# Kernel optimization log

Measured on AMD Instinct MI355X. Metric: run time of the kernel, lower is better.

Reference implementation:

```python
import jax, jax.numpy as jnp
import numpy as np

D_MODEL = 512; D_STATE = 32; D_HEAD = 64; G = 4; R = 2
D_INNER = 2 * D_MODEL            # expand=2 -> 1024
H = D_INNER // D_HEAD            # 16 heads
RATIO = H // G                   # 4 heads per group
CHUNK = 128; EPS = 1e-5
DIM_Z = D_INNER; DIM_X = D_INNER
DIM_B = G * D_STATE * R; DIM_C = DIM_B
D_PROJ = DIM_Z + DIM_X + DIM_B + DIM_C + G + G
BATCH = 1; SEQ = 2048


def setup_inputs() -> dict:
    key = jax.random.key(0)
    ks = jax.random.split(key, 10)
    u = jax.random.normal(ks[0], (BATCH, SEQ, D_MODEL), jnp.float32)
    W_in = jax.random.normal(ks[1], (D_MODEL, D_PROJ), jnp.float32) * 0.02
    b_in = jnp.zeros((D_PROJ,), jnp.float32)
    # dt bias init: inverse-softplus of log-uniform dt in [1e-3, 1e-1]
    dt0 = jnp.exp(jax.random.uniform(ks[2], (G,)) * (np.log(0.1) - np.log(0.001)) + np.log(0.001))
    inv_dt = dt0 + jnp.log(-jnp.expm1(-dt0))
    s = DIM_Z + DIM_X + DIM_B + DIM_C
    b_in = b_in.at[s:s + G].set(inv_dt).at[s + G:].set(-3.0)
    W_xup = jax.random.normal(ks[3], (D_HEAD, D_HEAD * R), jnp.float32) * (1.0 / np.sqrt(D_HEAD * R))
    W_ydown = jax.random.normal(ks[4], (D_HEAD * R, D_HEAD), jnp.float32) * (1.0 / np.sqrt(D_HEAD * R))
    A_log = jnp.log(jax.random.uniform(ks[5], (G,), minval=1.0, maxval=16.0))
    theta_log = jax.random.normal(ks[6], (G, D_STATE // 2), jnp.float32)
    D_param = jnp.ones((H,), jnp.float32)
    wB = jnp.ones((D_STATE * R,), jnp.float32)
    wC = jnp.ones((D_STATE * R,), jnp.float32)
    bias_B = jnp.ones((G, D_STATE, R), jnp.float32)
    bias_C = jnp.ones((G, D_STATE, R), jnp.float32)
    W_out = jax.random.normal(ks[7], (D_INNER, D_MODEL), jnp.float32) * 0.02
    return dict(u=u, W_in=W_in, b_in=b_in, W_xup=W_xup, W_ydown=W_ydown,
                A_log=A_log, theta_log=theta_log, D_param=D_param,
                wB=wB, wC=wC, bias_B=bias_B, bias_C=bias_C, W_out=W_out)


def rmsnorm(x, w):
    return x * jax.lax.rsqrt(jnp.mean(x * x, -1, keepdims=True) + EPS) * w


def apply_rope(x, angles):
    # x: (B,L,G,N,R)  angles: (B,L,G,N/2)  -- rotate (even, odd) pairs along N
    Bz, L, Gg, N, Rr = x.shape
    xr = x.reshape(Bz, L, Gg, N // 2, 2, Rr)
    re, im = xr[..., 0, :], xr[..., 1, :]
    c = jnp.cos(angles)[..., None]
    s = jnp.sin(angles)[..., None]
    out = jnp.stack([re * c - im * s, re * s + im * c], axis=-2)
    return out.reshape(Bz, L, Gg, N, Rr)


def segsum(x):
    # x: (..., T) log-decay -> (..., T, T) causal pairwise cumulative sums
    T = x.shape[-1]
    cs = jnp.cumsum(x, -1)
    seg = cs[..., :, None] - cs[..., None, :]
    mask = jnp.tril(jnp.ones((T, T), bool))
    return jnp.where(mask, seg, -jnp.inf)


def chunk_parallel_scan(u_in, dt, A, C):
    # u_in: (B,L,H,N,P)  dt: (B,L,H)  A: (H,)  C: (B,L,H,N,R)
    Bz, L, Hh, N, P = u_in.shape
    Rr = C.shape[-1]
    nc = L // CHUNK
    la = (dt * A).reshape(Bz, nc, CHUNK, Hh)                       # log alpha per chunk
    uc = u_in.reshape(Bz, nc, CHUNK, Hh, N, P)
    Cc = C.reshape(Bz, nc, CHUNK, Hh, N, Rr)
    Lm = jnp.exp(segsum(la.transpose(0, 1, 3, 2)))                 # (B,nc,H,cs,cs)
    h_intra = jnp.einsum('bchts,bcshnp->bcthnp', Lm, uc)           # intra-chunk states
    y_diag = jnp.einsum('bcthnp,bcthnr->bcthpr', h_intra, Cc)
    decay_chunk = jnp.exp(la.sum(2))                               # (B,nc,H)
    h_final = h_intra[:, :, -1]                                    # (B,nc,H,N,P)
    h0 = jnp.zeros((Bz, Hh, N, P), u_in.dtype)

    def step(h, inp):
        d, c = inp
        return h * d[..., None, None] + c, h

    h_last, h_states = jax.lax.scan(
        step, h0, (decay_chunk.transpose(1, 0, 2), h_final.transpose(1, 0, 2, 3, 4)))
    h_states = h_states.transpose(1, 0, 2, 3, 4)                   # state entering each chunk
    decay_intra = jnp.exp(jnp.cumsum(la, 2))                       # (B,nc,cs,H)
    C_scaled = Cc * decay_intra[..., None, None]
    y_off = jnp.einsum('bchnp,bcthnr->bcthpr', h_states, C_scaled)
    y = (y_diag + y_off).reshape(Bz, L, Hh, P, Rr)
    return y, h_last


def _forward(u, W_in, b_in, W_xup, W_ydown, A_log, theta_log, D_param, wB, wC, bias_B, bias_C, W_out):
    Bz, L, _ = u.shape
    N, P = D_STATE, D_HEAD
    proj = u @ W_in + b_in
    o = 0
    z = proj[..., o:o + DIM_Z]; o += DIM_Z
    x = proj[..., o:o + DIM_X]; o += DIM_X
    Bi = proj[..., o:o + DIM_B]; o += DIM_B
    Ci = proj[..., o:o + DIM_C]; o += DIM_C
    dt_raw = proj[..., o:o + G]; o += G
    lam_raw = proj[..., o:o + G]

    dt = jax.nn.softplus(dt_raw)                                   # (B,L,G)
    lam = jax.nn.sigmoid(lam_raw)                                  # trapezoidal coeff
    x = jax.nn.silu(x)

    Bm = rmsnorm(Bi.reshape(Bz, L, G, N * R), wB).reshape(Bz, L, G, N, R) + bias_B
    Cm = rmsnorm(Ci.reshape(Bz, L, G, N * R), wC).reshape(Bz, L, G, N, R) + bias_C

    # data-dependent RoPE: cumulative angles = cumsum_t(dt_t * theta)
    theta = jnp.exp(theta_log)                                     # (G, N/2)
    angles = jnp.cumsum(dt[..., None] * theta, axis=1)             # (B,L,G,N/2)
    Br = apply_rope(Bm, angles)
    Cr = apply_rope(Cm, angles)

    # expand group-shared dynamics to heads
    Bh = jnp.repeat(Br, RATIO, axis=2)                             # (B,L,H,N,R)
    Ch = jnp.repeat(Cr, RATIO, axis=2)
    dth = jnp.repeat(dt, RATIO, axis=2)                            # (B,L,H)
    lamh = jnp.repeat(lam, RATIO, axis=2)
    Ah = jnp.repeat(-jnp.exp(A_log), RATIO)                        # (H,)

    xh = x.reshape(Bz, L, H, P)
    x_up = (xh @ W_xup).reshape(Bz, L, H, P, R)                    # MIMO up-projection
    u_ssm = jnp.einsum('blhnr,blhpr->blhnp', Bh, x_up) * dth[..., None, None]
    # generalized trapezoidal rule: blend current and previous input contribution
    u_prev = jnp.pad(u_ssm[:, :-1], ((0, 0), (1, 0), (0, 0), (0, 0), (0, 0)))
    w = lamh[..., None, None]
    u_trap = w * u_ssm + (1.0 - w) * u_prev

    y, _h = chunk_parallel_scan(u_trap, dth, Ah, Ch)               # (B,L,H,P,R)
    y = y.reshape(Bz, L, H, P * R) @ W_ydown                       # MIMO down-projection
    y = y + D_param[None, None, :, None] * xh                      # skip connection
    y = y * jax.nn.silu(z.reshape(Bz, L, H, P))                    # gate
    return (y.reshape(Bz, L, D_INNER)) @ W_out


def reference(u, W_in, b_in, W_xup, W_ydown, A_log, theta_log, D_param, wB, wC, bias_B, bias_C, W_out):
    return _forward(u, W_in, b_in, W_xup, W_ydown, A_log, theta_log,
                    D_param, wB, wC, bias_B, bias_C, W_out)
```

## Files before the change

kernel.cpp:

```cpp
#include <hip/hip_runtime.h>
#include <hip/hip_bf16.h>

typedef __hip_bfloat16 bf16;
typedef __bf16 bfv8 __attribute__((ext_vector_type(8)));
typedef float fv4 __attribute__((ext_vector_type(4)));

__device__ __forceinline__ float bf2f(bf16 x){ return __bfloat162float(x); }
__device__ __forceinline__ bf16 f2bf(float x){ return __float2bfloat16(x); }
__device__ __forceinline__ float blo(unsigned u){ return __uint_as_float(u<<16); }
__device__ __forceinline__ float bhi(unsigned u){ return __uint_as_float(u & 0xffff0000u); }
struct __align__(8) bf4v { bf16 x,y,z,w; };
struct __align__(16) bf8s { ushort u[8]; };
__device__ __forceinline__ float4 ldb4(const bf16* p){
  ushort4 u = *(const ushort4*)p;
  float4 r;
  r.x = __uint_as_float(((unsigned)u.x)<<16);
  r.y = __uint_as_float(((unsigned)u.y)<<16);
  r.z = __uint_as_float(((unsigned)u.z)<<16);
  r.w = __uint_as_float(((unsigned)u.w)<<16);
  return r;
}
__device__ __forceinline__ void stb4(bf16* p, float4 v){
  bf4v t; t.x=f2bf(v.x); t.y=f2bf(v.y); t.z=f2bf(v.z); t.w=f2bf(v.w);
  *(bf4v*)p = t;
}

#define L_SEQ 2048
#define DPROJ 2568
#define NCHUNK 16
#define TCH 128

__device__ __forceinline__ void tbody(const float* __restrict__ in, bf16* __restrict__ out,
                                      int R, int C, int Cpad, int bx, int by, float (*t)[33])
{
  int c0 = bx*32, r0 = by*32;
  int tx = threadIdx.x & 31, ty = threadIdx.x >> 5;
  for (int i=0;i<32;i+=8){
    int r = r0+i+ty, cc = c0+tx;
    t[i+ty][tx] = (r<R && cc<C) ? in[(size_t)r*C+cc] : 0.f;
  }
  __syncthreads();
  for (int i=0;i<32;i+=8){
    int cc = c0+i+ty, r = r0+tx;
    if (cc<Cpad && r<R) out[(size_t)cc*R + r] = f2bf(t[tx][i+ty]);
  }
}

__global__ void prep(const float* __restrict__ u, bf16* __restrict__ ubf,
                     const float* __restrict__ Win, bf16* __restrict__ WinT,
                     const float* __restrict__ Wout, bf16* __restrict__ WoutT,
                     const float* __restrict__ Wyd, bf16* __restrict__ WydT,
                     const float* __restrict__ Wxup, bf16* __restrict__ WxupT)
{
  __shared__ float t[32][33];
  int b = blockIdx.x;
  if (b < 1024){
    int i = (b*256 + threadIdx.x)*4;
    float4 v = *(const float4*)&u[i];
    stb4(&ubf[i], v);
  } else if (b < 2368){
    int idx = b - 1024;
    tbody(Win, WinT, 512, DPROJ, 2688, idx%84, idx/84, t);
  } else if (b < 2880){
    int idx = b - 2368;
    tbody(Wout, WoutT, 1024, 512, 512, idx%16, idx/16, t);
  } else if (b < 2888){
    int idx = b - 2880;
    tbody(Wyd, WydT, 128, 64, 64, idx%2, idx/2, t);
  } else {
    int idx = b - 2888;
    tbody(Wxup, WxupT, 64, 128, 128, idx%4, idx/4, t);
  }
}

__global__ void __launch_bounds__(256) gemm1_mfma(const bf16* __restrict__ A, const bf16* __restrict__ BT,
                                                  const float* __restrict__ bias, bf16* __restrict__ C,
                                                  float* __restrict__ side)
{
  const int K = 512;
  __shared__ __align__(16) bf16 As[128*40];
  __shared__ __align__(16) bf16 Bs[128*40];
  int tid = threadIdx.x;
  int col0 = blockIdx.x*128, row0 = blockIdx.y*128;
  int wid = tid>>6, lane = tid&63;
  int wm = (wid&1)*64, wn = (wid>>1)*64;
  int lm = lane&15, lq = lane>>4;
  fv4 acc[4][4] = {};
  for (int k0=0;k0<K;k0+=32){
    #pragma unroll
    for (int i=0;i<2;i++){
      int e = tid + i*256;
      int r = e>>2, k8 = (e&3)*8;
      *(bf8s*)&As[r*40+k8] = *(const bf8s*)&A[(size_t)(row0+r)*K + k0 + k8];
      *(bf8s*)&Bs[r*40+k8] = *(const bf8s*)&BT[(size_t)(col0+r)*K + k0 + k8];
    }
    __syncthreads();
    bfv8 af[4], bfr[4];
    #pragma unroll
    for (int mf=0;mf<4;mf++) af[mf] = *(const bfv8*)&As[(wm+mf*16+lm)*40 + lq*8];
    #pragma unroll
    for (int nf=0;nf<4;nf++) bfr[nf] = *(const bfv8*)&Bs[(wn+nf*16+lm)*40 + lq*8];
    #pragma unroll
    for (int mf=0;mf<4;mf++)
      #pragma unroll
      for (int nf=0;nf<4;nf++)
        acc[mf][nf] = __builtin_amdgcn_mfma_f32_16x16x32_bf16(af[mf], bfr[nf], acc[mf][nf], 0,0,0);
    __syncthreads();
  }
  #pragma unroll
  for (int mf=0;mf<4;mf++){
    #pragma unroll
    for (int nf=0;nf<4;nf++){
      int gcol = col0 + wn + nf*16 + lm;
      if (gcol < DPROJ){
        float bia = bias[gcol];
        #pragma unroll
        for (int r=0;r<4;r++){
          int grow = row0 + wm + mf*16 + lq*4 + r;
          float v = acc[mf][nf][r] + bia;
          C[(size_t)grow*DPROJ + gcol] = f2bf(v);
          if (gcol >= 2560) side[grow*8 + (gcol-2560)] = v;
        }
      }
    }
  }
}

__global__ void __launch_bounds__(256) gemmo_mfma(const bf16* __restrict__ Yp, const bf16* __restrict__ BT,
                                                  float* __restrict__ C)
{
  const int K = 1024;
  __shared__ __align__(16) bf16 As[64*40];
  __shared__ __align__(16) bf16 Bs[64*40];
  int tid = threadIdx.x;
  int col0 = blockIdx.x*64, row0 = blockIdx.y*64;
  int wid = tid>>6, lane = tid&63;
  int wm = (wid&1)*32, wn = (wid>>1)*32;
  int lm = lane&15, lq = lane>>4;
  fv4 acc[2][2] = {};
  for (int k0=0;k0<K;k0+=32){
    {
      int m = tid>>2, k8 = (tid&3)*8;
      int kg = k0 + k8;
      *(bf8s*)&As[m*40+k8] = *(const bf8s*)&Yp[(size_t)(row0+m)*2048 + ((kg>>6)*128) + 64 + (kg&63)];
    }
    {
      int n = tid>>2, k8 = (tid&3)*8;
      *(bf8s*)&Bs[n*40+k8] = *(const bf8s*)&BT[(size_t)(col0+n)*K + k0 + k8];
    }
    __syncthreads();
    bfv8 af[2], bfr[2];
    #pragma unroll
    for (int mf=0;mf<2;mf++) af[mf] = *(const bfv8*)&As[(wm+mf*16+lm)*40 + lq*8];
    #pragma unroll
    for (int nf=0;nf<2;nf++) bfr[nf] = *(const bfv8*)&Bs[(wn+nf*16+lm)*40 + lq*8];
    #pragma unroll
    for (int mf=0;mf<2;mf++)
      #pragma unroll
      for (int nf=0;nf<2;nf++)
        acc[mf][nf] = __builtin_amdgcn_mfma_f32_16x16x32_bf16(af[mf], bfr[nf], acc[mf][nf], 0,0,0);
    __syncthreads();
  }
  #pragma unroll
  for (int mf=0;mf<2;mf++)
    #pragma unroll
    for (int nf=0;nf<2;nf++){
      int gcol = col0 + wn + nf*16 + lm;
      #pragma unroll
      for (int r=0;r<4;r++){
        int grow = row0 + wm + mf*16 + lq*4 + r;
        C[(size_t)grow*512 + gcol] = acc[mf][nf][r];
      }
    }
}

__global__ void k23(const float* __restrict__ dlraw, float* __restrict__ dtb,
                    float* __restrict__ lamb, float* __restrict__ csdt)
{
  __shared__ float raw[L_SEQ*8];
  __shared__ float dts[L_SEQ*4];
  __shared__ float segs[4][64];
  int tid = threadIdx.x;
  for (int e=tid;e<L_SEQ*8;e+=256) raw[e] = dlraw[e];
  __syncthreads();
  int g = tid & 3, seg = tid >> 2;
  for (int i = 0; i < 32; i++){
    int l = seg*32 + i;
    float dr = raw[l*8 + g];
    float lr = raw[l*8 + 4 + g];
    float dt = (dr > 15.f) ? dr : log1pf(__expf(dr));
    dts[l*4+g] = dt;
    dtb[l*4+g] = dt;
    lamb[l*4+g] = 1.f/(1.f+__expf(-lr));
  }
  __syncthreads();
  float s = 0.f;
  for (int i=0;i<32;i++) s += dts[(seg*32+i)*4 + g];
  segs[g][seg] = s;
  __syncthreads();
  if (tid < 4) { float run = 0.f; for (int q=0;q<64;q++){ float t = segs[tid][q]; segs[tid][q] = run; run += t; } }
  __syncthreads();
  float run = segs[g][seg];
  for (int i=0;i<32;i++){ int l = seg*32+i; run += dts[l*4+g]; csdt[l*4+g] = run; }
}

__global__ void __launch_bounds__(256) k45b(
  const bf16* __restrict__ proj, const float* __restrict__ wB, const float* __restrict__ wC,
  const float* __restrict__ biasB, const float* __restrict__ biasC,
  const float* __restrict__ theta_log, const float* __restrict__ csdt,
  bf16* __restrict__ Br, bf16* __restrict__ Cr)
{
  int tid = threadIdx.x;
  int g = tid >> 6, idx = tid & 63;
  int k = idx >> 2;
  bool is_im = (idx >> 1) & 1;
  float th = __expf(theta_log[g*16+k]);
  float wBv = wB[idx], wCv = wC[idx];
  float bBv = biasB[g*64+idx], bCv = biasC[g*64+idx];
  #pragma unroll
  for (int i=0;i<8;i++){
    int l = blockIdx.x*8 + i;
    const bf16* pr = proj + (size_t)l*DPROJ;
    float bv = bf2f(pr[2048 + g*64 + idx]);
    float cv = bf2f(pr[2304 + g*64 + idx]);
    float sb = bv*bv, sc = cv*cv;
    #pragma unroll
    for (int off=32; off; off>>=1){ sb += __shfl_xor(sb, off); sc += __shfl_xor(sc, off); }
    float rb = rsqrtf(sb*(1.f/64.f) + 1e-5f);
    float rc = rsqrtf(sc*(1.f/64.f) + 1e-5f);
    float bm = bv*rb*wBv + bBv;
    float cm = cv*rc*wCv + bCv;
    float ang = csdt[l*4+g] * th;
    float ca = cosf(ang), sa = sinf(ang);
    float bp = __shfl_xor(bm, 2);
    float cp = __shfl_xor(cm, 2);
    float bo = is_im ? (bp*sa + bm*ca) : (bm*ca - bp*sa);
    float co = is_im ? (cp*sa + cm*ca) : (cm*ca - cp*sa);
    Br[((size_t)l*4+g)*64 + idx] = f2bf(bo);
    Cr[((size_t)l*4+g)*64 + idx] = f2bf(co);
  }
}

__global__ void __launch_bounds__(256) xupg(
  const bf16* __restrict__ proj, const bf16* __restrict__ WxupT, bf16* __restrict__ xup)
{
  __shared__ __align__(16) bf16 As[128*72];
  __shared__ __align__(16) bf16 Bs[128*72];
  int tid = threadIdx.x;
  int m0 = blockIdx.x*128;
  for (int e = tid; e < 1024; e += 256){
    int n = e>>3, k8 = (e&7)*8;
    *(bf8s*)&Bs[n*72 + k8] = *(const bf8s*)&WxupT[n*64 + k8];
  }
  for (int e = tid; e < 1024; e += 256){
    int r = e>>3, k8 = (e&7)*8;
    int m = m0 + r;
    int l = m >> 4, h = m & 15;
    bf8s v = *(const bf8s*)&proj[(size_t)l*DPROJ + 1024 + h*64 + k8];
    float s[8];
    #pragma unroll
    for (int j=0;j<8;j++){
      float x = blo((unsigned)v.u[j]);
      s[j] = x/(1.f+__expf(-x));
    }
    stb4(&As[r*72 + k8],     make_float4(s[0],s[1],s[2],s[3]));
    stb4(&As[r*72 + k8 + 4], make_float4(s[4],s[5],s[6],s[7]));
  }
  __syncthreads();
  int wid = tid>>6, lane = tid&63;
  int wm = (wid&1)*64, wn = (wid>>1)*64;
  int lm = lane&15, lq = lane>>4;
  fv4 acc[4][4] = {};
  #pragma unroll
  for (int kk=0;kk<64;kk+=32){
    bfv8 af[4], bfr[4];
    #pragma unroll
    for (int mf=0;mf<4;mf++) af[mf] = *(const bfv8*)&As[(wm+mf*16+lm)*72 + kk + lq*8];
    #pragma unroll
    for (int nf=0;nf<4;nf++) bfr[nf] = *(const bfv8*)&Bs[(wn+nf*16+lm)*72 + kk + lq*8];
    #pragma unroll
    for (int mf=0;mf<4;mf++)
      #pragma unroll
      for (int nf=0;nf<4;nf++)
        acc[mf][nf] = __builtin_amdgcn_mfma_f32_16x16x32_bf16(af[mf], bfr[nf], acc[mf][nf], 0,0,0);
  }
  #pragma unroll
  for (int mf=0;mf<4;mf++)
    #pragma unroll
    for (int nf=0;nf<4;nf++){
      int col = wn + nf*16 + lm;
      #pragma unroll
      for (int r=0;r<4;r++){
        int m = m0 + wm + mf*16 + lq*4 + r;
        xup[(size_t)m*128 + col] = f2bf(acc[mf][nf][r]);
      }
    }
}

__global__ void __launch_bounds__(256) k6y(
  const bf16* __restrict__ Br, const bf16* __restrict__ Cr, const bf16* __restrict__ xup,
  const float* __restrict__ dtb, const float* __restrict__ lamb, const float* __restrict__ A_log,
  bf16* __restrict__ ypr, bf16* __restrict__ hfin, float* __restrict__ dcb, float* __restrict__ csb)
{
  __shared__ __align__(16) bf16 Cs[64*40];
  __shared__ __align__(16) bf16 Bs[64*40];
  __shared__ __align__(16) bf16 Bsn[32*72];
  __shared__ __align__(16) bf16 Fs[64*72];
  __shared__ __align__(16) bf16 Xs[64*72];
  __shared__ float dt_l[128], lam_l[128], cs_l[128];
  __shared__ float u1s[160], u12s[160], vs_[32];
  int bx = blockIdx.x; int g = bx & 3, q = bx >> 2;
  int c = blockIdx.y;
  int h4 = blockIdx.z;
  int h = g*4 + h4;
  int tid = threadIdx.x;
  int l0 = c*TCH;
  int w = tid>>6, lane = tid&63, lm = lane&15, lq = lane>>4;
  float Ah = -__expf(A_log[g]);
  float dt_prev = (c>0) ? dtb[(l0-1)*4+g] : 0.f;
  if (tid<128){ dt_l[tid] = dtb[(l0+tid)*4+g]; lam_l[tid] = lamb[(l0+tid)*4+g]; }
  __syncthreads();
  if (tid<128) cs_l[tid] = dt_l[tid]*Ah;
  __syncthreads();
  for (int off=1; off<128; off<<=1){
    float add = 0.f;
    if (tid<128 && tid>=off) add = cs_l[tid-off];
    __syncthreads();
    if (tid<128) cs_l[tid] += add;
    __syncthreads();
  }
  float ref = cs_l[q*32+16];
  if (tid < 160){
    int jj = tid;
    float u1v = 0.f, u2v = 0.f;
    if (jj>=1 && jj<=128) u1v = lam_l[jj-1]*dt_l[jj-1]*__expf(fminf(ref-cs_l[jj-1],60.f));
    if (jj<=127){ float dtx = (jj>=1)? dt_l[jj-1] : dt_prev; u2v = (1.f-lam_l[jj])*dtx*__expf(fminf(ref-cs_l[jj],60.f)); }
    u1s[jj] = u1v; u12s[jj] = u1v+u2v;
  }
  if (tid < 32) vs_[tid] = __expf(fminf(cs_l[q*32+tid]-ref,60.f));
  for (int e4 = tid; e4 < 512; e4 += 256){
    int tl = e4>>4, c4 = (e4&15)*4;
    bf4v v = *(const bf4v*)&Cr[((size_t)(l0+q*32+tl)*4+g)*64 + c4];
    bf16 arr[4] = {v.x,v.y,v.z,v.w};
    #pragma unroll
    for (int i=0;i<4;i++){ int q6=c4+i; Cs[((tl<<1)|(q6&1))*40 + (q6>>1)] = arr[i]; }
  }
  __syncthreads();
  float vfin = __expf(fminf(cs_l[127]-ref,60.f));
  fv4 acc[4] = {};
  fv4 acch[2] = {};
  int nch = (q+2 < 5) ? (q+2) : 5;
  for (int kc=0; kc<nch; kc++){
    for (int e4 = tid; e4 < 512; e4 += 256){
      int jjloc = e4>>4, c4 = (e4&15)*4;
      int jj = kc*32 + jjloc; int l = l0-1+jj;
      bf4v v;
      if (l >= 0 && jj <= 128) v = *(const bf4v*)&Br[((size_t)l*4+g)*64 + c4];
      else { v.x=v.y=v.z=v.w = f2bf(0.f); }
      bf16 arr[4] = {v.x,v.y,v.z,v.w};
      #pragma unroll
      for (int i=0;i<4;i++){ int q6=c4+i; Bs[((q6&1)*32+jjloc)*40 + (q6>>1)] = arr[i]; }
      if (q == 3){
        float gcv = vfin * u12s[jj];
        #pragma unroll
        for (int i=0;i<4;i++){ int q6=c4+i; Bsn[(q6>>1)*72 + (q6&1)*32 + jjloc] = f2bf(gcv*bf2f(arr[i])); }
      }
    }
    for (int e4 = tid; e4 < 1024; e4 += 256){
      int jjloc = e4>>5, c4 = (e4&31)*4;
      int jj = kc*32+jjloc; int l = l0-1+jj;
      bf4v v;
      if (l>=0 && jj<=128) v = *(const bf4v*)&xup[((size_t)l*16 + h)*128 + c4];
      else { v.x=v.y=v.z=v.w = f2bf(0.f); }
      bf16 arr[4] = {v.x,v.y,v.z,v.w};
      #pragma unroll
      for (int i=0;i<4;i++){ int q7=c4+i; Xs[(q7>>1)*72 + (q7&1)*32 + jjloc] = arr[i]; }
    }
    __syncthreads();
    {
      bfv8 a = *(const bfv8*)&Cs[(w*16+lm)*40 + lq*8];
      fv4 zz = {0.f,0.f,0.f,0.f};
      int rb = w*16 + lq*4;
      float vA = vs_[rb>>1];
      float vB = vs_[(rb>>1)+1];
      #pragma unroll
      for (int nt=0;nt<4;nt++){
        bfv8 b = *(const bfv8*)&Bs[(nt*16+lm)*40 + lq*8];
        fv4 s = __builtin_amdgcn_mfma_f32_16x16x32_bf16(a, b, zz, 0,0,0);
        int col = nt*16+lm;
        int jj = kc*32 + (col&31);
        float u1v = u1s[jj], u12v = u12s[jj];
        #pragma unroll
        for (int r=0;r<4;r++){
          int row = rb + r;
          float vT = (r<2) ? vA : vB;
          float cf;
          if (kc < q) cf = u12v;
          else {
            int T = q*32 + (row>>1);
            if (kc == q) cf = (jj<=T) ? u12v : ((jj==T+1) ? u1v : 0.f);
            else         cf = (jj==T+1) ? u1v : 0.f;
          }
          Fs[row*72+col] = f2bf(cf*vT*s[r]);
        }
      }
    }
    __syncthreads();
    #pragma unroll
    for (int r2=0;r2<2;r2++){
      bfv8 a = *(const bfv8*)&Fs[(w*16+lm)*72 + r2*32 + lq*8];
      #pragma unroll
      for (int nt=0;nt<4;nt++){
        bfv8 b = *(const bfv8*)&Xs[(nt*16+lm)*72 + r2*32 + lq*8];
        acc[nt] = __builtin_amdgcn_mfma_f32_16x16x32_bf16(a, b, acc[nt], 0,0,0);
      }
    }
    if (q == 3){
      #pragma unroll
      for (int r2=0;r2<2;r2++){
        bfv8 a = *(const bfv8*)&Xs[(w*16+lm)*72 + r2*32 + lq*8];
        #pragma unroll
        for (int nt2=0;nt2<2;nt2++){
          bfv8 b = *(const bfv8*)&Bsn[(nt2*16+lm)*72 + r2*32 + lq*8];
          acch[nt2] = __builtin_amdgcn_mfma_f32_16x16x32_bf16(a, b, acch[nt2], 0,0,0);
        }
      }
    }
    __syncthreads();
  }
  #pragma unroll
  for (int nt=0;nt<4;nt++){
    int p = nt*16+lm;
    #pragma unroll
    for (int r=0;r<4;r++){
      int row = w*16+lq*4+r;
      int T = q*32+(row>>1), r1 = row&1;
      ypr[((size_t)(l0+T)*16 + h)*128 + p*2+r1] = f2bf(acc[nt][r]);
    }
  }
  if (q == 3){
    #pragma unroll
    for (int nt2=0;nt2<2;nt2++){
      int n = nt2*16+lm;
      #pragma unroll
      for (int r=0;r<4;r++){
        int p = w*16+lq*4+r;
        hfin[(((size_t)c*16+h)*64 + p)*32 + n] = f2bf(acch[nt2][r]);
      }
    }
    if (tid == 0) dcb[c*16+h] = __expf(cs_l[127]);
  }
  if (q == 0 && h4 == 0 && tid < 128) csb[(c*4+g)*128 + tid] = cs_l[tid];
}

__global__ void __launch_bounds__(256) k8af(
  const bf16* __restrict__ Cr, const bf16* __restrict__ hfin,
  const float* __restrict__ dcb, const float* __restrict__ csb,
  bf16* __restrict__ ypr, const bf16* __restrict__ WydT,
  const bf16* __restrict__ proj, const float* __restrict__ Dp)
{
  __shared__ __align__(16) char arena[52224];
  bf16* C2s = (bf16*)arena;
  bf16* hT  = (bf16*)(arena + 20480);
  float* cse = (float*)(arena + 25600);
  bf16* Yf  = (bf16*)arena;
  bf16* Wds = (bf16*)(arena + 34816);
  int h = blockIdx.x, c = blockIdx.y;
  int g = h >> 2;
  int tid = threadIdx.x;
  int l0 = c*TCH;
  int w = tid>>6, lane = tid&63, lm = lane&15, lq = lane>>4;
  for (int e4 = tid; e4 < 2048; e4 += 256){
    int tl = e4>>4, c4 = (e4&15)*4;
    bf4v v = *(const bf4v*)&Cr[((size_t)(l0+tl)*4+g)*64 + c4];
    bf16 arr[4] = {v.x,v.y,v.z,v.w};
    #pragma unroll
    for (int i=0;i<4;i++){ int q6=c4+i; C2s[((tl<<1)|(q6&1))*40 + (q6>>1)] = arr[i]; }
  }
  for (int e = tid; e < 1024; e += 256){
    int qq = e>>4, k8 = (e&15)*8;
    *(bf8s*)&Wds[qq*136 + k8] = *(const bf8s*)&WydT[qq*128 + k8];
  }
  {
    int e0 = tid*8;
    float carry[8] = {};
    for (int j = 0; j < c; j++){
      float dc = dcb[j*16+h];
      float4 a = ldb4(&hfin[((size_t)j*16+h)*2048 + e0]);
      float4 b = ldb4(&hfin[((size_t)j*16+h)*2048 + e0 + 4]);
      carry[0]=carry[0]*dc+a.x; carry[1]=carry[1]*dc+a.y; carry[2]=carry[2]*dc+a.z; carry[3]=carry[3]*dc+a.w;
      carry[4]=carry[4]*dc+b.x; carry[5]=carry[5]*dc+b.y; carry[6]=carry[6]*dc+b.z; carry[7]=carry[7]*dc+b.w;
    }
    int p = e0>>5, n = e0&31;
    stb4(&hT[p*40+n],   make_float4(carry[0],carry[1],carry[2],carry[3]));
    stb4(&hT[p*40+n+4], make_float4(carry[4],carry[5],carry[6],carry[7]));
  }
  if (tid < 128) cse[tid] = __expf(csb[(c*4+g)*128 + tid]);
  __syncthreads();
  float yfull[4][4][4];
  fv4 zz = {0.f,0.f,0.f,0.f};
  #pragma unroll
  for (int mi=0;mi<4;mi++){
    int mt = w*4 + mi;
    bfv8 a = *(const bfv8*)&C2s[(mt*16+lm)*40 + lq*8];
    #pragma unroll
    for (int nt=0;nt<4;nt++){
      bfv8 b = *(const bfv8*)&hT[(nt*16+lm)*40 + lq*8];
      fv4 s = __builtin_amdgcn_mfma_f32_16x16x32_bf16(a, b, zz, 0,0,0);
      int p = nt*16+lm;
      #pragma unroll
      for (int r=0;r<4;r++){
        int row = mt*16+lq*4+r;
        int tl = row>>1, r1 = row&1;
        float yd = bf2f(ypr[((size_t)(l0+tl)*16 + h)*128 + p*2 + r1]);
        yfull[mi][nt][r] = yd + cse[tl]*s[r];
      }
    }
  }
  __syncthreads();
  #pragma unroll
  for (int mi=0;mi<4;mi++){
    int mt = w*4 + mi;
    #pragma unroll
    for (int nt=0;nt<4;nt++){
      int p = nt*16+lm;
      #pragma unroll
      for (int r=0;r<4;r++){
        int row = mt*16+lq*4+r;
        int tl = row>>1, r1 = row&1;
        Yf[tl*136 + p*2 + r1] = f2bf(yfull[mi][nt][r]);
      }
    }
  }
  __syncthreads();
  fv4 acc2[2][4] = {};
  #pragma unroll
  for (int kq=0;kq<4;kq++){
    #pragma unroll
    for (int m2=0;m2<2;m2++){
      bfv8 a = *(const bfv8*)&Yf[((w*2+m2)*16+lm)*136 + kq*32 + lq*8];
      #pragma unroll
      for (int nt2=0;nt2<4;nt2++){
        bfv8 b = *(const bfv8*)&Wds[(nt2*16+lm)*136 + kq*32 + lq*8];
        acc2[m2][nt2] = __builtin_amdgcn_mfma_f32_16x16x32_bf16(a, b, acc2[m2][nt2], 0,0,0);
      }
    }
  }
  float dv = Dp[h];
  #pragma unroll
  for (int m2=0;m2<2;m2++){
    #pragma unroll
    for (int nt2=0;nt2<4;nt2++){
      int qq = nt2*16+lm;
      #pragma unroll
      for (int r=0;r<4;r++){
        int tl = (w*2+m2)*16 + lq*4 + r;
        size_t lrow = (size_t)(l0+tl)*DPROJ;
        float x = bf2f(proj[lrow + 1024 + h*64 + qq]);
        float z = bf2f(proj[lrow + h*64 + qq]);
        float xs = x/(1.f+__expf(-x));
        float zs = z/(1.f+__expf(-z));
        float outv = (acc2[m2][nt2][r] + dv*xs)*zs;
        ypr[((size_t)(l0+tl)*16 + h)*128 + 64 + qq] = f2bf(outv);
      }
    }
  }
}

extern "C" void kernel_launch(void* const* d_in, const int* in_sizes, int n_in,
                              void* d_out, int out_size, void* d_ws, size_t ws_size,
                              hipStream_t stream) {
  const float* u       = (const float*)d_in[0];
  const float* W_in    = (const float*)d_in[1];
  const float* b_in    = (const float*)d_in[2];
  const float* W_xup   = (const float*)d_in[3];
  const float* W_ydown = (const float*)d_in[4];
  const float* A_log   = (const float*)d_in[5];
  const float* theta_l = (const float*)d_in[6];
  const float* D_p     = (const float*)d_in[7];
  const float* wB      = (const float*)d_in[8];
  const float* wC      = (const float*)d_in[9];
  const float* biasB   = (const float*)d_in[10];
  const float* biasC   = (const float*)d_in[11];
  const float* W_out   = (const float*)d_in[12];
  float* out = (float*)d_out;

  char* w = (char*)d_ws;
  bf16*  proj  = (bf16*)(w);
  float* dlraw = (float*)(w + 10518528);
  float* dtb   = (float*)(w + 10584064);
  float* lamb  = (float*)(w + 10616832);
  float* csdt  = (float*)(w + 10649600);
  bf16*  Brb   = (bf16*)(w + 10682368);
  bf16*  Crb   = (bf16*)(w + 11730944);
  bf16*  xupb  = (bf16*)(w + 12779520);
  bf16*  hfin  = (bf16*)(w + 21168128);
  bf16*  WxupT = (bf16*)(w + 22216704);
  float* dcb   = (float*)(w + 23265280);
  float* csb   = (float*)(w + 23266304);
  bf16*  ypr   = (bf16*)(w + 23299072);
  bf16*  WinT  = (bf16*)(w + 23299072);
  bf16*  ubf   = (bf16*)(w + 31687680);
  bf16*  WoutT = (bf16*)(w + 33784832);
  bf16*  WydT  = (bf16*)(w + 34833408);

  prep<<<2896,256,0,stream>>>(u, ubf, W_in, WinT, W_out, WoutT, W_ydown, WydT, W_xup, WxupT);
  gemm1_mfma<<<dim3(21,16),256,0,stream>>>(ubf, WinT, b_in, proj, dlraw);
  k23<<<1,256,0,stream>>>(dlraw, dtb, lamb, csdt);
  xupg<<<256,256,0,stream>>>(proj, WxupT, xupb);
  k45b<<<256,256,0,stream>>>(proj, wB, wC, biasB, biasC, theta_l, csdt, Brb, Crb);
  k6y<<<dim3(16,16,4),256,0,stream>>>(Brb, Crb, xupb, dtb, lamb, A_log, ypr, hfin, dcb, csb);
  k8af<<<dim3(16,16),256,0,stream>>>(Crb, hfin, dcb, csb, ypr, WydT, proj, D_p);
  gemmo_mfma<<<dim3(8,32),256,0,stream>>>(ypr, WoutT, out);
}
```

Before: 203.1 us.

## Fuse u conversion into GEMM, merge xup/BC kernels, deepen K tiles, shuffle scan

Drops the separate fp32-to-bf16 conversion of u and converts it inside the input-projection GEMM's shared-memory load. Widens the K step of both GEMMs (64 and 128) so there are fewer barrier round trips. Merges the x up-projection and B/C norm+RoPE kernels into one launch split by block index, and replaces the barrier-heavy shared-memory prefix scan in k6y with a wave shuffle scan. Together these cut launches, barriers and a global round trip, but use more LDS per block, which may lower occupancy.

```diff
diff --git a/kernel.cpp b/kernel.cpp
--- a/kernel.cpp
+++ b/kernel.cpp
@@ -46,65 +46,65 @@
   }
 }
 
-__global__ void prep(const float* __restrict__ u, bf16* __restrict__ ubf,
-                     const float* __restrict__ Win, bf16* __restrict__ WinT,
+__global__ void prep(const float* __restrict__ Win, bf16* __restrict__ WinT,
                      const float* __restrict__ Wout, bf16* __restrict__ WoutT,
                      const float* __restrict__ Wyd, bf16* __restrict__ WydT,
                      const float* __restrict__ Wxup, bf16* __restrict__ WxupT)
 {
   __shared__ float t[32][33];
   int b = blockIdx.x;
-  if (b < 1024){
-    int i = (b*256 + threadIdx.x)*4;
-    float4 v = *(const float4*)&u[i];
-    stb4(&ubf[i], v);
-  } else if (b < 2368){
-    int idx = b - 1024;
-    tbody(Win, WinT, 512, DPROJ, 2688, idx%84, idx/84, t);
-  } else if (b < 2880){
-    int idx = b - 2368;
+  if (b < 1344){
+    tbody(Win, WinT, 512, DPROJ, 2688, b%84, b/84, t);
+  } else if (b < 1856){
+    int idx = b - 1344;
     tbody(Wout, WoutT, 1024, 512, 512, idx%16, idx/16, t);
-  } else if (b < 2888){
-    int idx = b - 2880;
+  } else if (b < 1864){
+    int idx = b - 1856;
     tbody(Wyd, WydT, 128, 64, 64, idx%2, idx/2, t);
   } else {
-    int idx = b - 2888;
+    int idx = b - 1864;
     tbody(Wxup, WxupT, 64, 128, 128, idx%4, idx/4, t);
   }
 }
 
-__global__ void __launch_bounds__(256) gemm1_mfma(const bf16* __restrict__ A, const bf16* __restrict__ BT,
+__global__ void __launch_bounds__(256) gemm1_mfma(const float* __restrict__ A, const bf16* __restrict__ BT,
                                                   const float* __restrict__ bias, bf16* __restrict__ C,
                                                   float* __restrict__ side)
 {
   const int K = 512;
-  __shared__ __align__(16) bf16 As[128*40];
-  __shared__ __align__(16) bf16 Bs[128*40];
+  __shared__ __align__(16) bf16 As[128*72];
+  __shared__ __align__(16) bf16 Bs[128*72];
   int tid = threadIdx.x;
   int col0 = blockIdx.x*128, row0 = blockIdx.y*128;
   int wid = tid>>6, lane = tid&63;
   int wm = (wid&1)*64, wn = (wid>>1)*64;
   int lm = lane&15, lq = lane>>4;
   fv4 acc[4][4] = {};
-  for (int k0=0;k0<K;k0+=32){
-    #pragma unroll
-    for (int i=0;i<2;i++){
+  for (int k0=0;k0<K;k0+=64){
+    #pragma unroll
+    for (int i=0;i<4;i++){
       int e = tid + i*256;
-      int r = e>>2, k8 = (e&3)*8;
-      *(bf8s*)&As[r*40+k8] = *(const bf8s*)&A[(size_t)(row0+r)*K + k0 + k8];
-      *(bf8s*)&Bs[r*40+k8] = *(const bf8s*)&BT[(size_t)(col0+r)*K + k0 + k8];
-    }
-    __syncthreads();
-    bfv8 af[4], bfr[4];
-    #pragma unroll
-    for (int mf=0;mf<4;mf++) af[mf] = *(const bfv8*)&As[(wm+mf*16+lm)*40 + lq*8];
-    #pragma unroll
-    for (int nf=0;nf<4;nf++) bfr[nf] = *(const bfv8*)&Bs[(wn+nf*16+lm)*40 + lq*8];
-    #pragma unroll
-    for (int mf=0;mf<4;mf++)
-      #pragma unroll
-      for (int nf=0;nf<4;nf++)
-        acc[mf][nf] = __builtin_amdgcn_mfma_f32_16x16x32_bf16(af[mf], bfr[nf], acc[mf][nf], 0,0,0);
+      int r = e>>3, k8 = (e&7)*8;
+      float4 a0 = *(const float4*)&A[(size_t)(row0+r)*K + k0 + k8];
+      float4 a1 = *(const float4*)&A[(size_t)(row0+r)*K + k0 + k8 + 4];
+      stb4(&As[r*72+k8],   a0);
+      stb4(&As[r*72+k8+4], a1);
+      *(bf8s*)&Bs[r*72+k8] = *(const bf8s*)&BT[(size_t)(col0+r)*K + k0 + k8];
+    }
+    __syncthreads();
+    #pragma unroll
+    for (int ks=0;ks<2;ks++){
+      bfv8 af[4], bfr[4];
+      #pragma unroll
+      for (int mf=0;mf<4;mf++) af[mf] = *(const bfv8*)&As[(wm+mf*16+lm)*72 + ks*32 + lq*8];
+      #pragma unroll
+      for (int nf=0;nf<4;nf++) bfr[nf] = *(const bfv8*)&Bs[(wn+nf*16+lm)*72 + ks*32 + lq*8];
+      #pragma unroll
+      for (int mf=0;mf<4;mf++)
+        #pragma unroll
+        for (int nf=0;nf<4;nf++)
+          acc[mf][nf] = __builtin_amdgcn_mfma_f32_16x16x32_bf16(af[mf], bfr[nf], acc[mf][nf], 0,0,0);
+    }
     __syncthreads();
   }
   #pragma unroll
@@ -130,35 +130,37 @@
                                                   float* __restrict__ C)
 {
   const int K = 1024;
-  __shared__ __align__(16) bf16 As[64*40];
-  __shared__ __align__(16) bf16 Bs[64*40];
+  __shared__ __align__(16) bf16 As[64*136];
+  __shared__ __align__(16) bf16 Bs[64*136];
   int tid = threadIdx.x;
   int col0 = blockIdx.x*64, row0 = blockIdx.y*64;
   int wid = tid>>6, lane = tid&63;
   int wm = (wid&1)*32, wn = (wid>>1)*32;
   int lm = lane&15, lq = lane>>4;
   fv4 acc[2][2] = {};
-  for (int k0=0;k0<K;k0+=32){
-    {
-      int m = tid>>2, k8 = (tid&3)*8;
+  for (int k0=0;k0<K;k0+=128){
+    #pragma unroll
+    for (int i=0;i<4;i++){
+      int e = tid + i*256;
+      int m = e>>4, k8 = (e&15)*8;
       int kg = k0 + k8;
-      *(bf8s*)&As[m*40+k8] = *(const bf8s*)&Yp[(size_t)(row0+m)*2048 + ((kg>>6)*128) + 64 + (kg&63)];
-    }
-    {
-      int n = tid>>2, k8 = (tid&3)*8;
-      *(bf8s*)&Bs[n*40+k8] = *(const bf8s*)&BT[(size_t)(col0+n)*K + k0 + k8];
-    }
-    __syncthreads();
-    bfv8 af[2], bfr[2];
-    #pragma unroll
-    for (int mf=0;mf<2;mf++) af[mf] = *(const bfv8*)&As[(wm+mf*16+lm)*40 + lq*8];
-    #pragma unroll
-    for (int nf=0;nf<2;nf++) bfr[nf] = *(const bfv8*)&Bs[(wn+nf*16+lm)*40 + lq*8];
-    #pragma unroll
-    for (int mf=0;mf<2;mf++)
-      #pragma unroll
-      for (int nf=0;nf<2;nf++)
-        acc[mf][nf] = __builtin_amdgcn_mfma_f32_16x16x32_bf16(af[mf], bfr[nf], acc[mf][nf], 0,0,0);
+      *(bf8s*)&As[m*136+k8] = *(const bf8s*)&Yp[(size_t)(row0+m)*2048 + ((kg>>6)*128) + 64 + (kg&63)];
+      *(bf8s*)&Bs[m*136+k8] = *(const bf8s*)&BT[(size_t)(col0+m)*K + kg];
+    }
+    __syncthreads();
+    #pragma unroll
+    for (int ks=0;ks<4;ks++){
+      bfv8 af[2], bfr[2];
+      #pragma unroll
+      for (int mf=0;mf<2;mf++) af[mf] = *(const bfv8*)&As[(wm+mf*16+lm)*136 + ks*32 + lq*8];
+      #pragma unroll
+      for (int nf=0;nf<2;nf++) bfr[nf] = *(const bfv8*)&Bs[(wn+nf*16+lm)*136 + ks*32 + lq*8];
+      #pragma unroll
+      for (int mf=0;mf<2;mf++)
+        #pragma unroll
+        for (int nf=0;nf<2;nf++)
+          acc[mf][nf] = __builtin_amdgcn_mfma_f32_16x16x32_bf16(af[mf], bfr[nf], acc[mf][nf], 0,0,0);
+    }
     __syncthreads();
   }
   #pragma unroll
@@ -204,97 +206,95 @@
   for (int i=0;i<32;i++){ int l = seg*32+i; run += dts[l*4+g]; csdt[l*4+g] = run; }
 }
 
-__global__ void __launch_bounds__(256) k45b(
-  const bf16* __restrict__ proj, const float* __restrict__ wB, const float* __restrict__ wC,
+__global__ void __launch_bounds__(256) k45x(
+  const bf16* __restrict__ proj, const bf16* __restrict__ WxupT, bf16* __restrict__ xup,
+  const float* __restrict__ wB, const float* __restrict__ wC,
   const float* __restrict__ biasB, const float* __restrict__ biasC,
   const float* __restrict__ theta_log, const float* __restrict__ csdt,
   bf16* __restrict__ Br, bf16* __restrict__ Cr)
 {
-  int tid = threadIdx.x;
-  int g = tid >> 6, idx = tid & 63;
-  int k = idx >> 2;
-  bool is_im = (idx >> 1) & 1;
-  float th = __expf(theta_log[g*16+k]);
-  float wBv = wB[idx], wCv = wC[idx];
-  float bBv = biasB[g*64+idx], bCv = biasC[g*64+idx];
-  #pragma unroll
-  for (int i=0;i<8;i++){
-    int l = blockIdx.x*8 + i;
-    const bf16* pr = proj + (size_t)l*DPROJ;
-    float bv = bf2f(pr[2048 + g*64 + idx]);
-    float cv = bf2f(pr[2304 + g*64 + idx]);
-    float sb = bv*bv, sc = cv*cv;
-    #pragma unroll
-    for (int off=32; off; off>>=1){ sb += __shfl_xor(sb, off); sc += __shfl_xor(sc, off); }
-    float rb = rsqrtf(sb*(1.f/64.f) + 1e-5f);
-    float rc = rsqrtf(sc*(1.f/64.f) + 1e-5f);
-    float bm = bv*rb*wBv + bBv;
-    float cm = cv*rc*wCv + bCv;
-    float ang = csdt[l*4+g] * th;
-    float ca = cosf(ang), sa = sinf(ang);
-    float bp = __shfl_xor(bm, 2);
-    float cp = __shfl_xor(cm, 2);
-    float bo = is_im ? (bp*sa + bm*ca) : (bm*ca - bp*sa);
-    float co = is_im ? (cp*sa + cm*ca) : (cm*ca - cp*sa);
-    Br[((size_t)l*4+g)*64 + idx] = f2bf(bo);
-    Cr[((size_t)l*4+g)*64 + idx] = f2bf(co);
-  }
-}
-
-__global__ void __launch_bounds__(256) xupg(
-  const bf16* __restrict__ proj, const bf16* __restrict__ WxupT, bf16* __restrict__ xup)
-{
   __shared__ __align__(16) bf16 As[128*72];
   __shared__ __align__(16) bf16 Bs[128*72];
   int tid = threadIdx.x;
-  int m0 = blockIdx.x*128;
-  for (int e = tid; e < 1024; e += 256){
-    int n = e>>3, k8 = (e&7)*8;
-    *(bf8s*)&Bs[n*72 + k8] = *(const bf8s*)&WxupT[n*64 + k8];
-  }
-  for (int e = tid; e < 1024; e += 256){
-    int r = e>>3, k8 = (e&7)*8;
-    int m = m0 + r;
-    int l = m >> 4, h = m & 15;
-    bf8s v = *(const bf8s*)&proj[(size_t)l*DPROJ + 1024 + h*64 + k8];
-    float s[8];
-    #pragma unroll
-    for (int j=0;j<8;j++){
-      float x = blo((unsigned)v.u[j]);
-      s[j] = x/(1.f+__expf(-x));
-    }
-    stb4(&As[r*72 + k8],     make_float4(s[0],s[1],s[2],s[3]));
-    stb4(&As[r*72 + k8 + 4], make_float4(s[4],s[5],s[6],s[7]));
-  }
-  __syncthreads();
-  int wid = tid>>6, lane = tid&63;
-  int wm = (wid&1)*64, wn = (wid>>1)*64;
-  int lm = lane&15, lq = lane>>4;
-  fv4 acc[4][4] = {};
-  #pragma unroll
-  for (int kk=0;kk<64;kk+=32){
-    bfv8 af[4], bfr[4];
-    #pragma unroll
-    for (int mf=0;mf<4;mf++) af[mf] = *(const bfv8*)&As[(wm+mf*16+lm)*72 + kk + lq*8];
-    #pragma unroll
-    for (int nf=0;nf<4;nf++) bfr[nf] = *(const bfv8*)&Bs[(wn+nf*16+lm)*72 + kk + lq*8];
+  if (blockIdx.x < 256){
+    int m0 = blockIdx.x*128;
+    for (int e = tid; e < 1024; e += 256){
+      int n = e>>3, k8 = (e&7)*8;
+      *(bf8s*)&Bs[n*72 + k8] = *(const bf8s*)&WxupT[n*64 + k8];
+    }
+    for (int e = tid; e < 1024; e += 256){
+      int r = e>>3, k8 = (e&7)*8;
+      int m = m0 + r;
+      int l = m >> 4, h = m & 15;
+      bf8s v = *(const bf8s*)&proj[(size_t)l*DPROJ + 1024 + h*64 + k8];
+      float s[8];
+      #pragma unroll
+      for (int j=0;j<8;j++){
+        float x = blo((unsigned)v.u[j]);
+        s[j] = x/(1.f+__expf(-x));
+      }
+      stb4(&As[r*72 + k8],     make_float4(s[0],s[1],s[2],s[3]));
+      stb4(&As[r*72 + k8 + 4], make_float4(s[4],s[5],s[6],s[7]));
+    }
+    __syncthreads();
+    int wid = tid>>6, lane = tid&63;
+    int wm = (wid&1)*64, wn = (wid>>1)*64;
+    int lm = lane&15, lq = lane>>4;
+    fv4 acc[4][4] = {};
+    #pragma unroll
+    for (int kk=0;kk<64;kk+=32){
+      bfv8 af[4], bfr[4];
+      #pragma unroll
+      for (int mf=0;mf<4;mf++) af[mf] = *(const bfv8*)&As[(wm+mf*16+lm)*72 + kk + lq*8];
+      #pragma unroll
+      for (int nf=0;nf<4;nf++) bfr[nf] = *(const bfv8*)&Bs[(wn+nf*16+lm)*72 + kk + lq*8];
+      #pragma unroll
+      for (int mf=0;mf<4;mf++)
+        #pragma unroll
+        for (int nf=0;nf<4;nf++)
+          acc[mf][nf] = __builtin_amdgcn_mfma_f32_16x16x32_bf16(af[mf], bfr[nf], acc[mf][nf], 0,0,0);
+    }
     #pragma unroll
     for (int mf=0;mf<4;mf++)
       #pragma unroll
-      for (int nf=0;nf<4;nf++)
-        acc[mf][nf] = __builtin_amdgcn_mfma_f32_16x16x32_bf16(af[mf], bfr[nf], acc[mf][nf], 0,0,0);
-  }
-  #pragma unroll
-  for (int mf=0;mf<4;mf++)
-    #pragma unroll
-    for (int nf=0;nf<4;nf++){
-      int col = wn + nf*16 + lm;
-      #pragma unroll
-      for (int r=0;r<4;r++){
-        int m = m0 + wm + mf*16 + lq*4 + r;
-        xup[(size_t)m*128 + col] = f2bf(acc[mf][nf][r]);
-      }
-    }
+      for (int nf=0;nf<4;nf++){
+        int col = wn + nf*16 + lm;
+        #pragma unroll
+        for (int r=0;r<4;r++){
+          int m = m0 + wm + mf*16 + lq*4 + r;
+          xup[(size_t)m*128 + col] = f2bf(acc[mf][nf][r]);
+        }
+      }
+  } else {
+    int g = tid >> 6, idx = tid & 63;
+    int k = idx >> 2;
+    bool is_im = (idx >> 1) & 1;
+    float th = __expf(theta_log[g*16+k]);
+    float wBv = wB[idx], wCv = wC[idx];
+    float bBv = biasB[g*64+idx], bCv = biasC[g*64+idx];
+    #pragma unroll
+    for (int i=0;i<8;i++){
+      int l = (blockIdx.x-256)*8 + i;
+      const bf16* pr = proj + (size_t)l*DPROJ;
+      float bv = bf2f(pr[2048 + g*64 + idx]);
+      float cv = bf2f(pr[2304 + g*64 + idx]);
+      float sb = bv*bv, sc = cv*cv;
+      #pragma unroll
+      for (int off=32; off; off>>=1){ sb += __shfl_xor(sb, off); sc += __shfl_xor(sc, off); }
+      float rb = rsqrtf(sb*(1.f/64.f) + 1e-5f);
+      float rc = rsqrtf(sc*(1.f/64.f) + 1e-5f);
+      float bm = bv*rb*wBv + bBv;
+      float cm = cv*rc*wCv + bCv;
+      float ang = csdt[l*4+g] * th;
+      float ca = cosf(ang), sa = sinf(ang);
+      float bp = __shfl_xor(bm, 2);
+      float cp = __shfl_xor(cm, 2);
+      float bo = is_im ? (bp*sa + bm*ca) : (bm*ca - bp*sa);
+      float co = is_im ? (cp*sa + cm*ca) : (cm*ca - cp*sa);
+      Br[((size_t)l*4+g)*64 + idx] = f2bf(bo);
+      Cr[((size_t)l*4+g)*64 + idx] = f2bf(co);
+    }
+  }
 }
 
 __global__ void __launch_bounds__(256) k6y(
@@ -320,15 +320,18 @@
   float dt_prev = (c>0) ? dtb[(l0-1)*4+g] : 0.f;
   if (tid<128){ dt_l[tid] = dtb[(l0+tid)*4+g]; lam_l[tid] = lamb[(l0+tid)*4+g]; }
   __syncthreads();
-  if (tid<128) cs_l[tid] = dt_l[tid]*Ah;
-  __syncthreads();
-  for (int off=1; off<128; off<<=1){
-    float add = 0.f;
-    if (tid<128 && tid>=off) add = cs_l[tid-off];
-    __syncthreads();
-    if (tid<128) cs_l[tid] += add;
-    __syncthreads();
-  }
+  if (tid < 64){
+    float a = dt_l[2*tid]*Ah, b = dt_l[2*tid+1]*Ah;
+    float s = a + b;
+    #pragma unroll
+    for (int off=1; off<64; off<<=1){
+      float v = __shfl_up(s, off);
+      if (tid >= off) s += v;
+    }
+    cs_l[2*tid+1] = s;
+    cs_l[2*tid]   = s - b;
+  }
+  __syncthreads();
   float ref = cs_l[q*32+16];
   if (tid < 160){
     int jj = tid;
@@ -600,15 +603,13 @@
   float* csb   = (float*)(w + 23266304);
   bf16*  ypr   = (bf16*)(w + 23299072);
   bf16*  WinT  = (bf16*)(w + 23299072);
-  bf16*  ubf   = (bf16*)(w + 31687680);
   bf16*  WoutT = (bf16*)(w + 33784832);
   bf16*  WydT  = (bf16*)(w + 34833408);
 
-  prep<<<2896,256,0,stream>>>(u, ubf, W_in, WinT, W_out, WoutT, W_ydown, WydT, W_xup, WxupT);
-  gemm1_mfma<<<dim3(21,16),256,0,stream>>>(ubf, WinT, b_in, proj, dlraw);
+  prep<<<1872,256,0,stream>>>(W_in, WinT, W_out, WoutT, W_ydown, WydT, W_xup, WxupT);
+  gemm1_mfma<<<dim3(21,16),256,0,stream>>>(u, WinT, b_in, proj, dlraw);
   k23<<<1,256,0,stream>>>(dlraw, dtb, lamb, csdt);
-  xupg<<<256,256,0,stream>>>(proj, WxupT, xupb);
-  k45b<<<256,256,0,stream>>>(proj, wB, wC, biasB, biasC, theta_l, csdt, Brb, Crb);
+  k45x<<<512,256,0,stream>>>(proj, WxupT, xupb, wB, wC, biasB, biasC, theta_l, csdt, Brb, Crb);
   k6y<<<dim3(16,16,4),256,0,stream>>>(Brb, Crb, xupb, dtb, lamb, A_log, ypr, hfin, dcb, csb);
   k8af<<<dim3(16,16),256,0,stream>>>(Crb, hfin, dcb, csb, ypr, WydT, proj, D_p);
   gemmo_mfma<<<dim3(8,32),256,0,stream>>>(ypr, WoutT, out);
```

Result: faster. 191.2 us (-5.9%).
